# Kernel optimization log

Measured on AMD Instinct MI355X. Metric: run time of the kernel, lower is better.

## Reference

```python
import jax, jax.numpy as jnp
import numpy as np

M_FIELDS = 26   # cin_size[0]
H1 = 128        # cin_size[1]
H2 = 128        # cin_size[2]
BATCH = 2048
EMB_K = 32


def setup_inputs() -> dict:
    key = jax.random.key(0)
    k0, k1, k2, k3, k4 = jax.random.split(key, 5)
    inputs = jax.random.normal(k0, (BATCH, M_FIELDS, EMB_K), dtype=jnp.float32)
    # Conv3d(1, H1, kernel=(26,26,1)) -> weight [H1, H_prev=26, m=26], bias [H1]
    W1 = jax.random.normal(k1, (H1, M_FIELDS, M_FIELDS), dtype=jnp.float32) * 0.05
    b1 = jax.random.normal(k2, (H1,), dtype=jnp.float32) * 0.05
    # Conv3d(1, H2, kernel=(H1,26,1)) -> weight [H2, H1, m=26], bias [H2]
    W2 = jax.random.normal(k3, (H2, H1, M_FIELDS), dtype=jnp.float32) * 0.05
    b2 = jax.random.normal(k4, (H2,), dtype=jnp.float32) * 0.05
    return {"inputs": inputs, "W1": W1, "b1": b1, "W2": W2, "b2": b2}


def _cin_layer(x_prev, x0, W, b):
    # x_prev: [B, H_prev, k], x0: [B, m, k], W: [H, H_prev, m], b: [H]
    # Equivalent to: outer product z[b,i,j,k] = x_prev[b,i,k]*x0[b,j,k],
    # then Conv3d with kernel (H_prev, m, 1): out[b,h,k] = sum_ij W[h,i,j]*z + b[h]
    return jnp.einsum('bik,bjk,hij->bhk', x_prev, x0, W) + b[None, :, None]


def reference(inputs, W1, b1, W2, b2):
    x1 = _cin_layer(inputs, inputs, W1, b1)   # [B, H1, k]
    x2 = _cin_layer(x1, inputs, W2, b2)       # [B, H2, k]
    res = jnp.concatenate([x1, x2], axis=1)   # [B, H1+H2, k]
    return jnp.sum(res, axis=-1)              # [B, H1+H2]
```

## Files before the change

### kernel.cpp

```cpp
#include <hip/hip_runtime.h>

typedef __bf16 bf16;
typedef __bf16 bf16x8 __attribute__((ext_vector_type(8)));
typedef __bf16 bf16x4 __attribute__((ext_vector_type(4)));
typedef float f32x4 __attribute__((ext_vector_type(4)));
typedef unsigned int u32;

#define NB    2048
#define NM    26
#define NJP   27

__device__ __forceinline__ void gl_lds16(const bf16* g, bf16* l) {
  __builtin_amdgcn_global_load_lds(
      (const __attribute__((address_space(1))) void*)g,
      (__attribute__((address_space(3))) void*)l, 16, 0, 0);
}

__device__ __forceinline__ bf16x8 splat8(u32 p) {
  union { u32 u[4]; bf16x8 v; } s;
  s.u[0] = p; s.u[1] = p; s.u[2] = p; s.u[3] = p;
  return s.v;
}

__device__ __forceinline__ u32 dup16(float v) {
  union { bf16 h; unsigned short s; } cv; cv.h = (bf16)v;
  return (u32)cv.s * 0x10001u;
}

__global__ __launch_bounds__(256) void prep_all(
    const float* __restrict__ in, const float* __restrict__ W1,
    const float* __restrict__ W2,
    bf16* __restrict__ xb, bf16* __restrict__ w1t, bf16* __restrict__ w2t2)
{
  const int bid = blockIdx.x, t = threadIdx.x;
  if (bid < 8192) {
    int e = bid*256 + t;
    int row = e >> 5, j = e & 31;
    float v = (j < NM) ? in[(row >> 5)*(NM*32) + j*32 + (row & 31)] : 0.f;
    xb[e] = (bf16)v;
  } else if (bid < 8624) {
    int e = (bid-8192)*256 + t;
    int el = e & 7, lr = (e >> 3) & 15, lq = (e >> 7) & 3, ni = (e >> 9) & 3;
    int rest = e >> 11;
    int c = rest % NJP, cs_idx = rest / NJP;
    int h = cs_idx*64 + ni*16 + lr;
    int i = lq*8 + el;
    float v = (i < NM && c < NM) ? W1[h*(NM*NM) + i*NM + c] : 0.f;
    w1t[e] = (bf16)v;
  } else {
    int e = (bid-8624)*256 + t;
    int el = e & 7, lr = (e >> 3) & 15, lq = (e >> 7) & 3, ni = (e >> 9) & 3;
    int rest = e >> 11;
    int kc = rest % 130, cs_idx = rest / 130;
    int h = cs_idx*64 + ni*16 + lr;
    int c = lq*8 + el;
    float v = (kc < 128 && c < NM) ? W2[h*(128*NM) + kc*NM + c] : 0.f;
    w2t2[e] = (bf16)v;
  }
}

#define STEP(CUR, NXT, J) do {                                                 \
  __syncthreads();                                                             \
  gl_lds16(tb + (long)((J)+1)*2048 + t*8, &ldsB[NXT][t*8]);                    \
  { int jn = ((J)+1 > 25) ? 25 : (J)+1;         \
    sc[NXT][0] = dup16(spA[jn*32]);      sc[NXT][1] = dup16(spA[jn*32 + 16]);  \
    sc[NXT][2] = dup16(spB[jn*32]);      sc[NXT][3] = dup16(spB[jn*32 + 16]); }\
  bf16x8 bfr[4];                                                               \
  _Pragma("unroll")                                                            \
  for (int ni = 0; ni < 4; ++ni)                                               \
    bfr[ni] = *(const bf16x8*)&ldsB[CUR][ni*512 + fo];                         \
  _Pragma("unroll")                                                            \
  for (int mi = 0; mi < 4; ++mi) {                                             \
    bf16x8 af = xf[mi] * splat8(sc[CUR][mi]);                                  \
    _Pragma("unroll")                                                          \
    for (int ni = 0; ni < 4; ++ni)                                             \
      acc[mi][ni] = __builtin_amdgcn_mfma_f32_16x16x32_bf16(af, bfr[ni],       \
                                                            acc[mi][ni], 0, 0, 0); \
  }                                                                            \
} while (0)

__global__ __launch_bounds__(256, 4) void cin1G(
    const float* __restrict__ in, const bf16* __restrict__ xb,
    const bf16* __restrict__ w1t, const float* __restrict__ b1,
    bf16* __restrict__ G, float* __restrict__ out)
{
  __shared__ __align__(16) bf16 ldsB[2][2048];
  __shared__ __align__(16) bf16 ldsT[4][64*72];
  const int t = threadIdx.x;
  const int lane = t & 63, w = t >> 6;
  const int cs_idx = blockIdx.x & 1, cs = cs_idx * 64;
  const int strip4 = blockIdx.x >> 1;
  const int rowBase = strip4*256 + w*64;
  const int lr = lane & 15, lq = lane >> 4;
  const int fo = lq*128 + lr*8;
  const int b0 = rowBase >> 5;

  const float* spA = in + (long)b0*(NM*32) + lr;
  const float* spB = spA + NM*32;

  bf16x8 xf[4];
  #pragma unroll
  for (int mi = 0; mi < 4; ++mi)
    xf[mi] = *(const bf16x8*)&xb[(rowBase + mi*16 + lr)*32 + lq*8];

  f32x4 acc[4][4];
  #pragma unroll
  for (int mi=0; mi<4; ++mi)
    #pragma unroll
    for (int ni=0; ni<4; ++ni) acc[mi][ni] = {0.f,0.f,0.f,0.f};

  const bf16* tb = w1t + (long)cs_idx*NJP*2048;

  u32 sc[2][4];
  gl_lds16(tb + t*8, &ldsB[0][t*8]);
  sc[0][0] = dup16(spA[0]);  sc[0][1] = dup16(spA[16]);
  sc[0][2] = dup16(spB[0]);  sc[0][3] = dup16(spB[16]);

  for (int jj = 0; jj < 13; ++jj) {
    STEP(0, 1, 2*jj);
    STEP(1, 0, 2*jj + 1);
  }

  float bias[4];
  #pragma unroll
  for (int ni=0; ni<4; ++ni) bias[ni] = b1[cs + ni*16 + lr];

  #pragma unroll
  for (int half=0; half<2; ++half) {
    int b = b0 + half;
    #pragma unroll
    for (int ni=0; ni<4; ++ni) {
      float v = 0.f;
      #pragma unroll
      for (int mi=0; mi<2; ++mi)
        #pragma unroll
        for (int r=0; r<4; ++r) v += acc[half*2+mi][ni][r];
      v += __shfl_xor(v, 16, 64);
      v += __shfl_xor(v, 32, 64);
      if (lq == 0) out[b*256 + cs + ni*16 + lr] = v + 32.0f * bias[ni];
    }
  }

  bf16* T = &ldsT[w][0];
  #pragma unroll
  for (int mi=0; mi<4; ++mi)
    #pragma unroll
    for (int ni=0; ni<4; ++ni) {
      bf16x4 pk;
      #pragma unroll
      for (int r=0; r<4; ++r) pk[r] = (bf16)(acc[mi][ni][r] + bias[ni]);
      *(bf16x4*)&T[(ni*16+lr)*72 + mi*16 + lq*4] = pk;
    }

  #pragma unroll
  for (int h = 0; h < 2; ++h) {
    const int b = b0 + h;
    bf16x8 bg[2];
    #pragma unroll
    for (int nt = 0; nt < 2; ++nt) {
      int j = nt*16 + lr;
      bf16x8 v;
      #pragma unroll
      for (int e=0; e<8; ++e) v[e] = (bf16)0.f;
      if (j < NM) {
        const float* src = in + (long)b*(NM*32) + j*32 + lq*8;
        f32x4 a = *(const f32x4*)src, c = *(const f32x4*)(src+4);
        #pragma unroll
        for (int e=0; e<4; ++e) { v[e] = (bf16)a[e]; v[4+e] = (bf16)c[e]; }
      }
      bg[nt] = v;
    }
    #pragma unroll
    for (int mt = 0; mt < 4; ++mt) {
      bf16x8 ag = *(const bf16x8*)&T[(mt*16+lr)*72 + h*32 + lq*8];
      #pragma unroll
      for (int nt = 0; nt < 2; ++nt) {
        f32x4 z = {0.f,0.f,0.f,0.f};
        f32x4 g = __builtin_amdgcn_mfma_f32_16x16x32_bf16(ag, bg[nt], z, 0, 0, 0);
        #pragma unroll
        for (int r = 0; r < 4; ++r)
          G[(long)b*4096 + (cs + mt*16 + lq*4 + r)*32 + nt*16 + lr] = (bf16)g[r];
      }
    }
  }
}

#define STEPG(CUR, NXT, KN) do {                                               \
  _Pragma("unroll")                                                            \
  for (int mi = 0; mi < 2; ++mi)                                               \
    A[NXT][mi] = *(const bf16x8*)(Ab + (long)(mi*16+lr)*4096 + (KN)*32);       \
  _Pragma("unroll")                                                            \
  for (int ni = 0; ni < 4; ++ni)                                               \
    B[NXT][ni] = *(const bf16x8*)(tb + (long)(KN)*2048 + ni*512);              \
  _Pragma("unroll")                                                            \
  for (int mi = 0; mi < 2; ++mi)                                               \
    _Pragma("unroll")                                                          \
    for (int ni = 0; ni < 4; ++ni)                                             \
      acc[mi][ni] = __builtin_amdgcn_mfma_f32_16x16x32_bf16(A[CUR][mi],        \
                                  B[CUR][ni], acc[mi][ni], 0, 0, 0);           \
} while (0)

__global__ __launch_bounds__(256, 4) void gemm2(
    const bf16* __restrict__ G, const bf16* __restrict__ w2t2, float* __restrict__ p)
{
  const int t = threadIdx.x;
  const int lane = t & 63, w = t >> 6;
  const int s = blockIdx.x >> 5;
  const int q32 = blockIdx.x & 31;
  const int tile = q32*4 + w;
  const int cs_idx = tile & 1, ms = tile >> 1;
  const int rowB = ms*32;
  const int lr = lane & 15, lq = lane >> 4;
  const int fo = lq*128 + lr*8;
  const int kc0 = s*16;

  const bf16* Ab = G + (long)rowB*4096 + lq*8;
  const bf16* tb = w2t2 + (long)cs_idx*130*2048 + fo;

  f32x4 acc[2][4];
  #pragma unroll
  for (int mi=0; mi<2; ++mi)
    #pragma unroll
    for (int ni=0; ni<4; ++ni) acc[mi][ni] = {0.f,0.f,0.f,0.f};

  bf16x8 A[2][2], B[2][4];
  #pragma unroll
  for (int mi=0; mi<2; ++mi)
    A[0][mi] = *(const bf16x8*)(Ab + (long)(mi*16+lr)*4096 + kc0*32);
  #pragma unroll
  for (int ni=0; ni<4; ++ni)
    B[0][ni] = *(const bf16x8*)(tb + (long)kc0*2048 + ni*512);

  for (int jj = 0; jj < 8; ++jj) {
    STEPG(0, 1, kc0 + 2*jj + 1);
    STEPG(1, 0, kc0 + 2*jj + 2);
  }

  #pragma unroll
  for (int mi=0; mi<2; ++mi)
    #pragma unroll
    for (int ni=0; ni<4; ++ni) {
      int h = cs_idx*64 + ni*16 + lr;
      #pragma unroll
      for (int r=0; r<4; ++r) {
        int b = rowB + mi*16 + lq*4 + r;
        p[((long)s*NB + b)*128 + h] = acc[mi][ni][r];
      }
    }
}

__global__ __launch_bounds__(256) void combine(
    const float* __restrict__ p, const float* __restrict__ b2, float* __restrict__ out)
{
  int idx = blockIdx.x * 256 + threadIdx.x;
  int b = idx >> 7, h = idx & 127;
  float v = 32.0f * b2[h];
  #pragma unroll
  for (int s=0; s<8; ++s) v += p[((long)s*NB + b)*128 + h];
  out[b*256 + 128 + h] = v;
}

extern "C" void kernel_launch(void* const* d_in, const int* in_sizes, int n_in,
                              void* d_out, int out_size, void* d_ws, size_t ws_size,
                              hipStream_t stream) {
  const float* in = (const float*)d_in[0];
  const float* W1 = (const float*)d_in[1];
  const float* b1 = (const float*)d_in[2];
  const float* W2 = (const float*)d_in[3];
  const float* b2 = (const float*)d_in[4];
  float* out = (float*)d_out;

  char* ws = (char*)d_ws;
  bf16* xb   = (bf16*)(ws);
  bf16* w1t  = (bf16*)(ws + 4194304);
  bf16* w2t2 = (bf16*)(ws + 4415488);
  bf16* G    = (bf16*)(ws + 5480448);
  float* p   = (float*)(ws + 22257664);

  prep_all<<<10704, 256, 0, stream>>>(in, W1, W2, xb, w1t, w2t2);
  cin1G   <<<512,   256, 0, stream>>>(in, xb, w1t, b1, G, out);
  gemm2   <<<256,   256, 0, stream>>>(G, w2t2, p);
  combine <<<1024,  256, 0, stream>>>(p, b2, out);
}
```

Measured before the change: 112.6 us.

## Drop xb staging and combine kernel, retile G layout, use atomics for split-K

Removes the separate bf16 transpose of the input (cin1G now loads and converts its A fragments directly from fp32), halves per-wave batch work to one batch element with twice as many blocks, and rewrites G into a blocked layout so gemm2 A-fragment loads become contiguous. The split-K partial buffer and combine kernel are replaced by initializing the bias in prep_all and atomically adding gemm2 partials into the output. This cuts one launch and several global round trips, but adds float atomics, which make the summation order nondeterministic, and leaves cin1G with strided scalar loads.

```diff
diff --git a/kernel.cpp b/kernel.cpp
--- a/kernel.cpp
+++ b/kernel.cpp
@@ -28,18 +28,13 @@
 }
 
 __global__ __launch_bounds__(256) void prep_all(
-    const float* __restrict__ in, const float* __restrict__ W1,
-    const float* __restrict__ W2,
-    bf16* __restrict__ xb, bf16* __restrict__ w1t, bf16* __restrict__ w2t2)
+    const float* __restrict__ W1, const float* __restrict__ W2,
+    const float* __restrict__ b2,
+    bf16* __restrict__ w1t, bf16* __restrict__ w2t2, float* __restrict__ out)
 {
   const int bid = blockIdx.x, t = threadIdx.x;
-  if (bid < 8192) {
+  if (bid < 432) {
     int e = bid*256 + t;
-    int row = e >> 5, j = e & 31;
-    float v = (j < NM) ? in[(row >> 5)*(NM*32) + j*32 + (row & 31)] : 0.f;
-    xb[e] = (bf16)v;
-  } else if (bid < 8624) {
-    int e = (bid-8192)*256 + t;
     int el = e & 7, lr = (e >> 3) & 15, lq = (e >> 7) & 3, ni = (e >> 9) & 3;
     int rest = e >> 11;
     int c = rest % NJP, cs_idx = rest / NJP;
@@ -47,8 +42,8 @@
     int i = lq*8 + el;
     float v = (i < NM && c < NM) ? W1[h*(NM*NM) + i*NM + c] : 0.f;
     w1t[e] = (bf16)v;
-  } else {
-    int e = (bid-8624)*256 + t;
+  } else if (bid < 2512) {
+    int e = (bid-432)*256 + t;
     int el = e & 7, lr = (e >> 3) & 15, lq = (e >> 7) & 3, ni = (e >> 9) & 3;
     int rest = e >> 11;
     int kc = rest % 130, cs_idx = rest / 130;
@@ -56,6 +51,10 @@
     int c = lq*8 + el;
     float v = (kc < 128 && c < NM) ? W2[h*(128*NM) + kc*NM + c] : 0.f;
     w2t2[e] = (bf16)v;
+  } else {
+    int e = (bid-2512)*256 + t;
+    int b = e >> 7, h = e & 127;
+    out[b*256 + 128 + h] = 32.0f * b2[h];
   }
 }
 
@@ -63,14 +62,14 @@
   __syncthreads();                                                             \
   gl_lds16(tb + (long)((J)+1)*2048 + t*8, &ldsB[NXT][t*8]);                    \
   { int jn = ((J)+1 > 25) ? 25 : (J)+1;         \
-    sc[NXT][0] = dup16(spA[jn*32]);      sc[NXT][1] = dup16(spA[jn*32 + 16]);  \
-    sc[NXT][2] = dup16(spB[jn*32]);      sc[NXT][3] = dup16(spB[jn*32 + 16]); }\
+    sc[NXT][0] = dup16(spw[jn*32]);                                            \
+    sc[NXT][1] = dup16(spw[jn*32 + 16]); }                                     \
   bf16x8 bfr[4];                                                               \
   _Pragma("unroll")                                                            \
   for (int ni = 0; ni < 4; ++ni)                                               \
     bfr[ni] = *(const bf16x8*)&ldsB[CUR][ni*512 + fo];                         \
   _Pragma("unroll")                                                            \
-  for (int mi = 0; mi < 4; ++mi) {                                             \
+  for (int mi = 0; mi < 2; ++mi) {                                             \
     bf16x8 af = xf[mi] * splat8(sc[CUR][mi]);                                  \
     _Pragma("unroll")                                                          \
     for (int ni = 0; ni < 4; ++ni)                                             \
@@ -80,41 +79,42 @@
 } while (0)
 
 __global__ __launch_bounds__(256, 4) void cin1G(
-    const float* __restrict__ in, const bf16* __restrict__ xb,
-    const bf16* __restrict__ w1t, const float* __restrict__ b1,
-    bf16* __restrict__ G, float* __restrict__ out)
+    const float* __restrict__ in, const bf16* __restrict__ w1t,
+    const float* __restrict__ b1, bf16* __restrict__ G2, float* __restrict__ out)
 {
   __shared__ __align__(16) bf16 ldsB[2][2048];
-  __shared__ __align__(16) bf16 ldsT[4][64*72];
+  __shared__ __align__(16) bf16 ldsT[4][64*36];
   const int t = threadIdx.x;
   const int lane = t & 63, w = t >> 6;
   const int cs_idx = blockIdx.x & 1, cs = cs_idx * 64;
-  const int strip4 = blockIdx.x >> 1;
-  const int rowBase = strip4*256 + w*64;
+  const int strip = blockIdx.x >> 1;
+  const int bw = strip*4 + w;
   const int lr = lane & 15, lq = lane >> 4;
   const int fo = lq*128 + lr*8;
-  const int b0 = rowBase >> 5;
-
-  const float* spA = in + (long)b0*(NM*32) + lr;
-  const float* spB = spA + NM*32;
-
-  bf16x8 xf[4];
-  #pragma unroll
-  for (int mi = 0; mi < 4; ++mi)
-    xf[mi] = *(const bf16x8*)&xb[(rowBase + mi*16 + lr)*32 + lq*8];
-
-  f32x4 acc[4][4];
-  #pragma unroll
-  for (int mi=0; mi<4; ++mi)
+
+  const float* bin = in + (long)bw*(NM*32);
+  const float* spw = bin + lr;
+
+  bf16x8 xf[2];
+  #pragma unroll
+  for (int mi = 0; mi < 2; ++mi)
+    #pragma unroll
+    for (int e = 0; e < 8; ++e) {
+      int j = lq*8 + e;
+      xf[mi][e] = (bf16)((j < NM) ? bin[j*32 + mi*16 + lr] : 0.f);
+    }
+
+  f32x4 acc[2][4];
+  #pragma unroll
+  for (int mi=0; mi<2; ++mi)
     #pragma unroll
     for (int ni=0; ni<4; ++ni) acc[mi][ni] = {0.f,0.f,0.f,0.f};
 
   const bf16* tb = w1t + (long)cs_idx*NJP*2048;
 
-  u32 sc[2][4];
+  u32 sc[2][2];
   gl_lds16(tb + t*8, &ldsB[0][t*8]);
-  sc[0][0] = dup16(spA[0]);  sc[0][1] = dup16(spA[16]);
-  sc[0][2] = dup16(spB[0]);  sc[0][3] = dup16(spB[16]);
+  sc[0][0] = dup16(spw[0]);  sc[0][1] = dup16(spw[16]);
 
   for (int jj = 0; jj < 13; ++jj) {
     STEP(0, 1, 2*jj);
@@ -126,61 +126,57 @@
   for (int ni=0; ni<4; ++ni) bias[ni] = b1[cs + ni*16 + lr];
 
   #pragma unroll
-  for (int half=0; half<2; ++half) {
-    int b = b0 + half;
-    #pragma unroll
-    for (int ni=0; ni<4; ++ni) {
-      float v = 0.f;
-      #pragma unroll
-      for (int mi=0; mi<2; ++mi)
-        #pragma unroll
-        for (int r=0; r<4; ++r) v += acc[half*2+mi][ni][r];
-      v += __shfl_xor(v, 16, 64);
-      v += __shfl_xor(v, 32, 64);
-      if (lq == 0) out[b*256 + cs + ni*16 + lr] = v + 32.0f * bias[ni];
-    }
+  for (int ni=0; ni<4; ++ni) {
+    float v = 0.f;
+    #pragma unroll
+    for (int mi=0; mi<2; ++mi)
+      #pragma unroll
+      for (int r=0; r<4; ++r) v += acc[mi][ni][r];
+    v += __shfl_xor(v, 16, 64);
+    v += __shfl_xor(v, 32, 64);
+    if (lq == 0) out[bw*256 + cs + ni*16 + lr] = v + 32.0f * bias[ni];
   }
 
   bf16* T = &ldsT[w][0];
   #pragma unroll
-  for (int mi=0; mi<4; ++mi)
+  for (int mi=0; mi<2; ++mi)
     #pragma unroll
     for (int ni=0; ni<4; ++ni) {
       bf16x4 pk;
       #pragma unroll
       for (int r=0; r<4; ++r) pk[r] = (bf16)(acc[mi][ni][r] + bias[ni]);
-      *(bf16x4*)&T[(ni*16+lr)*72 + mi*16 + lq*4] = pk;
-    }
-
-  #pragma unroll
-  for (int h = 0; h < 2; ++h) {
-    const int b = b0 + h;
-    bf16x8 bg[2];
+      *(bf16x4*)&T[(ni*16+lr)*36 + mi*16 + lq*4] = pk;
+    }
+
+  bf16x8 bg[2];
+  #pragma unroll
+  for (int nt = 0; nt < 2; ++nt) {
+    int j = nt*16 + lr;
+    bf16x8 v;
+    #pragma unroll
+    for (int e=0; e<8; ++e) v[e] = (bf16)0.f;
+    if (j < NM) {
+      const float* src = bin + j*32 + lq*8;
+      f32x4 a = *(const f32x4*)src, c = *(const f32x4*)(src+4);
+      #pragma unroll
+      for (int e=0; e<4; ++e) { v[e] = (bf16)a[e]; v[4+e] = (bf16)c[e]; }
+    }
+    bg[nt] = v;
+  }
+  const long gbase = (long)(bw >> 5)*131072 + (bw & 31)*8;
+  #pragma unroll
+  for (int mt = 0; mt < 4; ++mt) {
+    bf16x8 ag = *(const bf16x8*)&T[(mt*16+lr)*36 + lq*8];
     #pragma unroll
     for (int nt = 0; nt < 2; ++nt) {
-      int j = nt*16 + lr;
-      bf16x8 v;
-      #pragma unroll
-      for (int e=0; e<8; ++e) v[e] = (bf16)0.f;
-      if (j < NM) {
-        const float* src = in + (long)b*(NM*32) + j*32 + lq*8;
-        f32x4 a = *(const f32x4*)src, c = *(const f32x4*)(src+4);
-        #pragma unroll
-        for (int e=0; e<4; ++e) { v[e] = (bf16)a[e]; v[4+e] = (bf16)c[e]; }
+      f32x4 z = {0.f,0.f,0.f,0.f};
+      f32x4 g = __builtin_amdgcn_mfma_f32_16x16x32_bf16(ag, bg[nt], z, 0, 0, 0);
+      const int jh = nt*2 + (lr >> 3), jl = lr & 7;
+      #pragma unroll
+      for (int r = 0; r < 4; ++r) {
+        int i = cs + mt*16 + lq*4 + r;
+        G2[gbase + (long)(i*4 + jh)*256 + jl] = (bf16)g[r];
       }
-      bg[nt] = v;
-    }
-    #pragma unroll
-    for (int mt = 0; mt < 4; ++mt) {
-      bf16x8 ag = *(const bf16x8*)&T[(mt*16+lr)*72 + h*32 + lq*8];
-      #pragma unroll
-      for (int nt = 0; nt < 2; ++nt) {
-        f32x4 z = {0.f,0.f,0.f,0.f};
-        f32x4 g = __builtin_amdgcn_mfma_f32_16x16x32_bf16(ag, bg[nt], z, 0, 0, 0);
-        #pragma unroll
-        for (int r = 0; r < 4; ++r)
-          G[(long)b*4096 + (cs + mt*16 + lq*4 + r)*32 + nt*16 + lr] = (bf16)g[r];
-      }
     }
   }
 }
@@ -188,7 +184,7 @@
 #define STEPG(CUR, NXT, KN) do {                                               \
   _Pragma("unroll")                                                            \
   for (int mi = 0; mi < 2; ++mi)                                               \
-    A[NXT][mi] = *(const bf16x8*)(Ab + (long)(mi*16+lr)*4096 + (KN)*32);       \
+    A[NXT][mi] = *(const bf16x8*)(Ab + (long)(KN)*1024 + mi*128);              \
   _Pragma("unroll")                                                            \
   for (int ni = 0; ni < 4; ++ni)                                               \
     B[NXT][ni] = *(const bf16x8*)(tb + (long)(KN)*2048 + ni*512);              \
@@ -201,7 +197,7 @@
 } while (0)
 
 __global__ __launch_bounds__(256, 4) void gemm2(
-    const bf16* __restrict__ G, const bf16* __restrict__ w2t2, float* __restrict__ p)
+    const bf16* __restrict__ G2, const bf16* __restrict__ w2t2, float* __restrict__ out)
 {
   const int t = threadIdx.x;
   const int lane = t & 63, w = t >> 6;
@@ -209,12 +205,11 @@
   const int q32 = blockIdx.x & 31;
   const int tile = q32*4 + w;
   const int cs_idx = tile & 1, ms = tile >> 1;
-  const int rowB = ms*32;
   const int lr = lane & 15, lq = lane >> 4;
   const int fo = lq*128 + lr*8;
   const int kc0 = s*16;
 
-  const bf16* Ab = G + (long)rowB*4096 + lq*8;
+  const bf16* Ab = G2 + ((long)(ms*512 + lq)*32 + lr)*8;
   const bf16* tb = w2t2 + (long)cs_idx*130*2048 + fo;
 
   f32x4 acc[2][4];
@@ -226,7 +221,7 @@
   bf16x8 A[2][2], B[2][4];
   #pragma unroll
   for (int mi=0; mi<2; ++mi)
-    A[0][mi] = *(const bf16x8*)(Ab + (long)(mi*16+lr)*4096 + kc0*32);
+    A[0][mi] = *(const bf16x8*)(Ab + (long)kc0*1024 + mi*128);
   #pragma unroll
   for (int ni=0; ni<4; ++ni)
     B[0][ni] = *(const bf16x8*)(tb + (long)kc0*2048 + ni*512);
@@ -243,21 +238,10 @@
       int h = cs_idx*64 + ni*16 + lr;
       #pragma unroll
       for (int r=0; r<4; ++r) {
-        int b = rowB + mi*16 + lq*4 + r;
-        p[((long)s*NB + b)*128 + h] = acc[mi][ni][r];
+        int b = ms*32 + mi*16 + lq*4 + r;
+        atomicAdd(&out[b*256 + 128 + h], acc[mi][ni][r]);
       }
     }
-}
-
-__global__ __launch_bounds__(256) void combine(
-    const float* __restrict__ p, const float* __restrict__ b2, float* __restrict__ out)
-{
-  int idx = blockIdx.x * 256 + threadIdx.x;
-  int b = idx >> 7, h = idx & 127;
-  float v = 32.0f * b2[h];
-  #pragma unroll
-  for (int s=0; s<8; ++s) v += p[((long)s*NB + b)*128 + h];
-  out[b*256 + 128 + h] = v;
 }
 
 extern "C" void kernel_launch(void* const* d_in, const int* in_sizes, int n_in,
@@ -271,14 +255,11 @@
   float* out = (float*)d_out;
 
   char* ws = (char*)d_ws;
-  bf16* xb   = (bf16*)(ws);
-  bf16* w1t  = (bf16*)(ws + 4194304);
-  bf16* w2t2 = (bf16*)(ws + 4415488);
-  bf16* G    = (bf16*)(ws + 5480448);
-  float* p   = (float*)(ws + 22257664);
-
-  prep_all<<<10704, 256, 0, stream>>>(in, W1, W2, xb, w1t, w2t2);
-  cin1G   <<<512,   256, 0, stream>>>(in, xb, w1t, b1, G, out);
-  gemm2   <<<256,   256, 0, stream>>>(G, w2t2, p);
-  combine <<<1024,  256, 0, stream>>>(p, b2, out);
-}
+  bf16* w1t  = (bf16*)(ws);
+  bf16* w2t2 = (bf16*)(ws + 1048576);
+  bf16* G2   = (bf16*)(ws + 4194304);
+
+  prep_all<<<3536, 256, 0, stream>>>(W1, W2, b2, w1t, w2t2, out);
+  cin1G   <<<1024, 256, 0, stream>>>(in, w1t, b1, G2, out);
+  gemm2   <<<256,  256, 0, stream>>>(G2, w2t2, out);
+}
```

Result: faster. 106.9 us (median of 2 runs) (-5.0%).
